# Optimization experiments

Measured on AMD Instinct MI355X. Metric: run time of the kernel, lower is better.

Reference implementation:

```python
import jax, jax.numpy as jnp
import numpy as np
from functools import partial

TAU = 2.0          # leak
VTH = 1.0          # threshold_value
DECAY = 1.0 - 1.0 / TAU  # decay_input=False, v_reset=0: v = v*(1-1/tau) + x
PAD = 3
STRIDE = 1


def heaviside(x):
    # forward of spikingjelly surrogate.ATan (surrogate only changes backward)
    return (x >= 0).astype(x.dtype)


def lif(v, inp):
    """One LIF step: charge, fire, hard reset (v_reset=0)."""
    v = v * DECAY + inp
    s = heaviside(v - VTH)
    v = v * (1.0 - s)
    return v, s


def setup_inputs() -> dict:
    key = jax.random.key(0)
    k1, k2, k3, k4 = jax.random.split(key, 4)
    B, L = 64, 2048
    C, H, NC, K = 128, 256, 10, 7
    x = jax.random.normal(k1, (B, L), dtype=jnp.float32)
    conv_w = jax.random.normal(k2, (C, 1, K), dtype=jnp.float32) * (1.0 / np.sqrt(K))
    W1 = jax.random.normal(k3, (H, C), dtype=jnp.float32) * (1.0 / np.sqrt(C))
    W2 = jax.random.normal(k4, (NC, H), dtype=jnp.float32) * (1.0 / np.sqrt(H))
    return {"x": x, "conv_w": conv_w, "W1": W1, "W2": W2}


def _forward(x, conv_w, W1, W2):
    B = x.shape[0]
    C, H, NC = conv_w.shape[0], W1.shape[0], W2.shape[0]
    # Conv1d(1 -> C): [B, 1, L] -> [B, C, T]
    xc = jax.lax.conv_general_dilated(
        x[:, None, :], conv_w, window_strides=(STRIDE,),
        padding=[(PAD, PAD)], dimension_numbers=("NCH", "OIH", "NCH"))
    T = xc.shape[2]
    xt = jnp.transpose(xc, (2, 0, 1))  # [T, B, C]

    def step(carry, x_t):
        v1, v2, v3, acc = carry
        v1, s1 = lif(v1, x_t)                       # conv LIF  [B, C]
        v2, s2 = lif(v2, s1 @ W1.T)                 # hidden LIF [B, H]
        v3, s3 = lif(v3, s2 @ W2.T)                 # output LIF [B, NC]
        return (v1, v2, v3, acc + s3), None

    zeros = lambda d: jnp.zeros((B, d), dtype=x.dtype)
    init = (zeros(C), zeros(H), zeros(NC), zeros(NC))
    (_, _, _, acc), _ = jax.lax.scan(step, init, xt)
    return acc / T


def reference(x, conv_w, W1, W2):
    return _forward(x, conv_w, W1, W2)
```

## Files before the change

### kernel.cpp

```cpp
#include <hip/hip_runtime.h>
#include <stdint.h>

#define T_STEPS 2048
#define BB 64
#define CC 128
#define HH 256
#define NCLS 10

#define S1_OFF  0
#define DP_OFF  16777216
#define DP2_OFF 16908288
#define S2B_OFF 16924672

typedef int v4i __attribute__((ext_vector_type(4)));

__global__ __launch_bounds__(128) void k01_prep(
    const float* __restrict__ x, const float* __restrict__ cw,
    const float* __restrict__ W1, const float* __restrict__ W2,
    unsigned char* __restrict__ s1, signed char* __restrict__ dp,
    signed char* __restrict__ dp2, float* __restrict__ out) {
  const int bx = blockIdx.x;
  const int tidx = threadIdx.x;

  if (bx < 1024) {
    const int c = tidx;
    const int b = bx & 63;
    const int t0 = (bx >> 6) * 128;
    const int ts = t0 - 64;

    float w[7];
#pragma unroll
    for (int k = 0; k < 7; ++k) w[k] = cw[c * 7 + k];

    const float* xb = x + b * 2048;
    float xw[7];
#pragma unroll
    for (int k = 0; k < 7; ++k) {
      int l = ts + k - 3;
      xw[k] = (l >= 0 && l < 2048) ? xb[l] : 0.0f;
    }

    float v = 0.0f;
#pragma unroll 7
    for (int t = ts; t < t0 + 128; ++t) {
      float u = fmaf(w[0], xw[0],
                fmaf(w[1], xw[1],
                fmaf(w[2], xw[2],
                fmaf(w[3], xw[3],
                fmaf(w[4], xw[4],
                fmaf(w[5], xw[5], w[6] * xw[6]))))));
      v = fmaf(v, 0.5f, u);
      bool sp = (v >= 1.0f);
      if (t >= t0) s1[((size_t)t * BB + b) * CC + c] = (unsigned char)(sp ? 1 : 0);
      if (sp) v = 0.0f;
#pragma unroll
      for (int k = 0; k < 6; ++k) xw[k] = xw[k + 1];
      int ln = t + 4;
      xw[6] = (ln >= 0 && ln < 2048) ? xb[ln] : 0.0f;
    }
  } else if (bx < 1280) {
    const int h = bx - 1024;
    const int c = tidx;
    float w = W1[h * CC + c];
    int q = __float2int_rn(w * 2147483648.0f);
#pragma unroll
    for (int d = 0; d < 3; ++d) {
      int dig = (int)(signed char)(q & 0xff);
      dp[d * (HH * CC) + h * CC + c] = (signed char)dig;
      q = (q - dig) >> 8;
    }
    dp[3 * (HH * CC) + h * CC + c] = (signed char)q;
  } else if (bx < 1296) {
    const int nc = bx - 1280;
#pragma unroll
    for (int half = 0; half < 2; ++half) {
      int cc = half * 128 + tidx;
      float w = (nc < NCLS) ? W2[nc * HH + cc] : 0.0f;
      int q = __float2int_rn(w * 2147483648.0f);
#pragma unroll
      for (int d = 0; d < 3; ++d) {
        int dig = (int)(signed char)(q & 0xff);
        dp2[d * (16 * HH) + nc * HH + cc] = (signed char)dig;
        q = (q - dig) >> 8;
      }
      dp2[3 * (16 * HH) + nc * HH + cc] = (signed char)q;
    }
  } else {
#pragma unroll
    for (int i = 0; i < 5; ++i) out[tidx + 128 * i] = 0.0f;
  }
}

__global__ __launch_bounds__(256, 4) void k2_mfma_lif2(
    const unsigned char* __restrict__ s1, const signed char* __restrict__ dp,
    unsigned char* __restrict__ s2b) {
  const int tid  = threadIdx.x;
  const int lane = tid & 63;
  const int wv   = tid >> 6;
  const int hg   = blockIdx.x;
  const int b    = blockIdx.y;
  const int chunk= blockIdx.z;
  const int t0   = chunk * 256;
  const int nwarm= (chunk == 0) ? 0 : 4;
  const int ts   = t0 - nwarm * 16;
  const int l15  = lane & 15;
  const int lg   = lane >> 4;
  const int h    = hg * 64 + wv * 16 + l15;

  v4i Bf[4][2];
#pragma unroll
  for (int d = 0; d < 4; ++d)
#pragma unroll
    for (int kc = 0; kc < 2; ++kc)
      Bf[d][kc] = *(const v4i*)(dp + d * (HH * CC) + h * CC + kc * 64 + lg * 16);

  const unsigned char* ap =
      s1 + ((size_t)(ts + l15) * BB + b) * CC + lg * 16;
  v4i Af0 = *(const v4i*)(ap);
  v4i Af1 = *(const v4i*)(ap + 64);
  ap += 16 * BB * CC;

  const int a4 = l15 * 4;
  float v = 0.0f;

  const int nsub = nwarm + 16;
  for (int s = 0; s < nsub; ++s) {
    const int tb = ts + s * 16;

    v4i Pf0 = *(const v4i*)(ap);
    v4i Pf1 = *(const v4i*)(ap + 64);
    ap += 16 * BB * CC;

    v4i a0 = {0, 0, 0, 0}, a1 = {0, 0, 0, 0}, a2 = {0, 0, 0, 0}, a3 = {0, 0, 0, 0};
    a0 = __builtin_amdgcn_mfma_i32_16x16x64_i8(Af0, Bf[0][0], a0, 0, 0, 0);
    a1 = __builtin_amdgcn_mfma_i32_16x16x64_i8(Af0, Bf[1][0], a1, 0, 0, 0);
    a2 = __builtin_amdgcn_mfma_i32_16x16x64_i8(Af0, Bf[2][0], a2, 0, 0, 0);
    a3 = __builtin_amdgcn_mfma_i32_16x16x64_i8(Af0, Bf[3][0], a3, 0, 0, 0);
    a0 = __builtin_amdgcn_mfma_i32_16x16x64_i8(Af1, Bf[0][1], a0, 0, 0, 0);
    a1 = __builtin_amdgcn_mfma_i32_16x16x64_i8(Af1, Bf[1][1], a1, 0, 0, 0);
    a2 = __builtin_amdgcn_mfma_i32_16x16x64_i8(Af1, Bf[2][1], a2, 0, 0, 0);
    a3 = __builtin_amdgcn_mfma_i32_16x16x64_i8(Af1, Bf[3][1], a3, 0, 0, 0);

    float u[4];
#pragma unroll
    for (int r = 0; r < 4; ++r) {
      int hi = a3[r] * 256 + a2[r];
      int lo = a1[r] * 256 + a0[r];
      u[r] = fmaf((float)hi, 0x1p-15f, (float)lo * 0x1p-31f);
    }

    float ua[4][4];
#pragma unroll
    for (int q = 0; q < 4; ++q) {
      const int addr = a4 + q * 64;
#pragma unroll
      for (int r = 0; r < 4; ++r)
        ua[q][r] = __int_as_float(
            __builtin_amdgcn_ds_bpermute(addr, __float_as_int(u[r])));
    }

    unsigned spbits = 0;
#pragma unroll
    for (int q = 0; q < 4; ++q)
#pragma unroll
      for (int r = 0; r < 4; ++r) {
        v = fmaf(v, 0.5f, ua[q][r]);
        bool sp = (v >= 1.0f);
        if (sp) v = 0.0f;
        spbits |= (sp ? 1u : 0u) << (q * 4 + r);
      }

    if (s >= nwarm) {
      size_t base = ((size_t)(tb + lg * 4) * BB + b) * 256 + h;
#pragma unroll
      for (int r = 0; r < 4; ++r)
        s2b[base + (size_t)r * (BB * 256)] =
            (unsigned char)((spbits >> (lg * 4 + r)) & 1u);
    }

    Af0 = Pf0; Af1 = Pf1;
  }
}

__global__ __launch_bounds__(64) void k34_gemm3_lif3(
    const unsigned char* __restrict__ s2b, const signed char* __restrict__ dp2,
    float* __restrict__ out) {
  const int lane = threadIdx.x;
  const int l15  = lane & 15;
  const int lg   = lane >> 4;
  const int b    = blockIdx.x;
  const int chunk= blockIdx.y;
  const int t0   = chunk * 64;
  const int nwarm= (chunk == 0) ? 0 : 4;
  const int ts   = t0 - nwarm * 16;

  v4i Bf[4][4];
#pragma unroll
  for (int d = 0; d < 4; ++d)
#pragma unroll
    for (int kc = 0; kc < 4; ++kc)
      Bf[d][kc] = *(const v4i*)(dp2 + d * (16 * HH) + l15 * HH + kc * 64 + lg * 16);

  const unsigned char* ap =
      s2b + ((size_t)(ts + l15) * BB + b) * 256 + lg * 16;
  v4i Af[4];
#pragma unroll
  for (int kc = 0; kc < 4; ++kc) Af[kc] = *(const v4i*)(ap + kc * 64);
  ap += 16 * BB * 256;

  const int a4 = l15 * 4;
  float v = 0.0f, cnt = 0.0f;
  const int nsub = nwarm + 4;
  for (int s = 0; s < nsub; ++s) {
    v4i Pf[4];
#pragma unroll
    for (int kc = 0; kc < 4; ++kc) Pf[kc] = *(const v4i*)(ap + kc * 64);
    ap += 16 * BB * 256;

    v4i a0 = {0, 0, 0, 0}, a1 = {0, 0, 0, 0}, a2 = {0, 0, 0, 0}, a3 = {0, 0, 0, 0};
#pragma unroll
    for (int kc = 0; kc < 4; ++kc) {
      a0 = __builtin_amdgcn_mfma_i32_16x16x64_i8(Af[kc], Bf[0][kc], a0, 0, 0, 0);
      a1 = __builtin_amdgcn_mfma_i32_16x16x64_i8(Af[kc], Bf[1][kc], a1, 0, 0, 0);
      a2 = __builtin_amdgcn_mfma_i32_16x16x64_i8(Af[kc], Bf[2][kc], a2, 0, 0, 0);
      a3 = __builtin_amdgcn_mfma_i32_16x16x64_i8(Af[kc], Bf[3][kc], a3, 0, 0, 0);
    }

    float u[4];
#pragma unroll
    for (int r = 0; r < 4; ++r) {
      int hi = a3[r] * 256 + a2[r];
      int lo = a1[r] * 256 + a0[r];
      u[r] = fmaf((float)hi, 0x1p-15f, (float)lo * 0x1p-31f);
    }

    float ua[4][4];
#pragma unroll
    for (int q = 0; q < 4; ++q) {
      const int addr = a4 + q * 64;
#pragma unroll
      for (int r = 0; r < 4; ++r)
        ua[q][r] = __int_as_float(
            __builtin_amdgcn_ds_bpermute(addr, __float_as_int(u[r])));
    }

    float inc = (s >= nwarm) ? 1.0f : 0.0f;
#pragma unroll
    for (int q = 0; q < 4; ++q)
#pragma unroll
      for (int r = 0; r < 4; ++r) {
        v = fmaf(v, 0.5f, ua[q][r]);
        bool sp = (v >= 1.0f);
        if (sp) { v = 0.0f; cnt += inc; }
      }

#pragma unroll
    for (int kc = 0; kc < 4; ++kc) Af[kc] = Pf[kc];
  }

  if (lane < NCLS)
    atomicAdd(&out[b * NCLS + lane], cnt * (1.0f / 2048.0f));
}

extern "C" void kernel_launch(void* const* d_in, const int* in_sizes, int n_in,
                              void* d_out, int out_size, void* d_ws, size_t ws_size,
                              hipStream_t stream) {
  const float* x  = (const float*)d_in[0];
  const float* cw = (const float*)d_in[1];
  const float* W1 = (const float*)d_in[2];
  const float* W2 = (const float*)d_in[3];
  float* out = (float*)d_out;

  char* ws = (char*)d_ws;
  unsigned char* s1  = (unsigned char*)(ws + S1_OFF);
  signed char*   dp  = (signed char*)(ws + DP_OFF);
  signed char*   dp2 = (signed char*)(ws + DP2_OFF);
  unsigned char* s2b = (unsigned char*)(ws + S2B_OFF);

  k01_prep<<<dim3(1297), 128, 0, stream>>>(x, cw, W1, W2, s1, dp, dp2, out);
  k2_mfma_lif2<<<dim3(4, 64, 8), 256, 0, stream>>>(s1, dp, s2b);
  k34_gemm3_lif3<<<dim3(64, 32), 64, 0, stream>>>(s2b, dp2, out);
  (void)in_sizes; (void)n_in; (void)out_size; (void)ws_size;
}
```

Before: 158.1 us.

## Bit-pack hidden-layer spikes and widen per-wave hidden tile in LIF2 kernel

The hidden spike tensor s2 is stored as packed 32-bit bitmasks built with wave ballots instead of one byte per neuron, which cuts the intermediate write and read traffic by eight times. Each wave in the LIF2 kernel now covers 32 hidden units using two MFMA column tiles, halving the grid in the hidden dimension. The output-layer kernel unpacks the bits back into int8 MFMA operands with multiply-mask tricks and uses shorter time chunks for more parallelism, which adds ALU work, more ballots and more warmup overhead relative to useful steps.

```diff
diff --git a/kernel.cpp b/kernel.cpp
--- a/kernel.cpp
+++ b/kernel.cpp
@@ -10,7 +10,7 @@
 #define S1_OFF  0
 #define DP_OFF  16777216
 #define DP2_OFF 16908288
-#define S2B_OFF 16924672
+#define S2W_OFF 16924672
 
 typedef int v4i __attribute__((ext_vector_type(4)));
 
@@ -93,7 +93,7 @@
 
 __global__ __launch_bounds__(256, 4) void k2_mfma_lif2(
     const unsigned char* __restrict__ s1, const signed char* __restrict__ dp,
-    unsigned char* __restrict__ s2b) {
+    unsigned int* __restrict__ s2w) {
   const int tid  = threadIdx.x;
   const int lane = tid & 63;
   const int wv   = tid >> 6;
@@ -105,14 +105,18 @@
   const int ts   = t0 - nwarm * 16;
   const int l15  = lane & 15;
   const int lg   = lane >> 4;
-  const int h    = hg * 64 + wv * 16 + l15;
-
-  v4i Bf[4][2];
-#pragma unroll
-  for (int d = 0; d < 4; ++d)
-#pragma unroll
-    for (int kc = 0; kc < 2; ++kc)
-      Bf[d][kc] = *(const v4i*)(dp + d * (HH * CC) + h * CC + kc * 64 + lg * 16);
+  const int nn   = lg >> 1;
+  const int hb   = hg * 128 + wv * 32;
+
+  v4i Bf[2][4][2];
+#pragma unroll
+  for (int n = 0; n < 2; ++n)
+#pragma unroll
+    for (int d = 0; d < 4; ++d)
+#pragma unroll
+      for (int kc = 0; kc < 2; ++kc)
+        Bf[n][d][kc] = *(const v4i*)(dp + d * (HH * CC) +
+                                     (hb + n * 16 + l15) * CC + kc * 64 + lg * 16);
 
   const unsigned char* ap =
       s1 + ((size_t)(ts + l15) * BB + b) * CC + lg * 16;
@@ -131,66 +135,67 @@
     v4i Pf1 = *(const v4i*)(ap + 64);
     ap += 16 * BB * CC;
 
-    v4i a0 = {0, 0, 0, 0}, a1 = {0, 0, 0, 0}, a2 = {0, 0, 0, 0}, a3 = {0, 0, 0, 0};
-    a0 = __builtin_amdgcn_mfma_i32_16x16x64_i8(Af0, Bf[0][0], a0, 0, 0, 0);
-    a1 = __builtin_amdgcn_mfma_i32_16x16x64_i8(Af0, Bf[1][0], a1, 0, 0, 0);
-    a2 = __builtin_amdgcn_mfma_i32_16x16x64_i8(Af0, Bf[2][0], a2, 0, 0, 0);
-    a3 = __builtin_amdgcn_mfma_i32_16x16x64_i8(Af0, Bf[3][0], a3, 0, 0, 0);
-    a0 = __builtin_amdgcn_mfma_i32_16x16x64_i8(Af1, Bf[0][1], a0, 0, 0, 0);
-    a1 = __builtin_amdgcn_mfma_i32_16x16x64_i8(Af1, Bf[1][1], a1, 0, 0, 0);
-    a2 = __builtin_amdgcn_mfma_i32_16x16x64_i8(Af1, Bf[2][1], a2, 0, 0, 0);
-    a3 = __builtin_amdgcn_mfma_i32_16x16x64_i8(Af1, Bf[3][1], a3, 0, 0, 0);
-
-    float u[4];
-#pragma unroll
-    for (int r = 0; r < 4; ++r) {
-      int hi = a3[r] * 256 + a2[r];
-      int lo = a1[r] * 256 + a0[r];
-      u[r] = fmaf((float)hi, 0x1p-15f, (float)lo * 0x1p-31f);
-    }
-
-    float ua[4][4];
+    float u0[4], u1[4];
+#pragma unroll
+    for (int n = 0; n < 2; ++n) {
+      v4i a0 = {0, 0, 0, 0}, a1 = {0, 0, 0, 0}, a2 = {0, 0, 0, 0}, a3 = {0, 0, 0, 0};
+      a0 = __builtin_amdgcn_mfma_i32_16x16x64_i8(Af0, Bf[n][0][0], a0, 0, 0, 0);
+      a1 = __builtin_amdgcn_mfma_i32_16x16x64_i8(Af0, Bf[n][1][0], a1, 0, 0, 0);
+      a2 = __builtin_amdgcn_mfma_i32_16x16x64_i8(Af0, Bf[n][2][0], a2, 0, 0, 0);
+      a3 = __builtin_amdgcn_mfma_i32_16x16x64_i8(Af0, Bf[n][3][0], a3, 0, 0, 0);
+      a0 = __builtin_amdgcn_mfma_i32_16x16x64_i8(Af1, Bf[n][0][1], a0, 0, 0, 0);
+      a1 = __builtin_amdgcn_mfma_i32_16x16x64_i8(Af1, Bf[n][1][1], a1, 0, 0, 0);
+      a2 = __builtin_amdgcn_mfma_i32_16x16x64_i8(Af1, Bf[n][2][1], a2, 0, 0, 0);
+      a3 = __builtin_amdgcn_mfma_i32_16x16x64_i8(Af1, Bf[n][3][1], a3, 0, 0, 0);
+#pragma unroll
+      for (int r = 0; r < 4; ++r) {
+        int hi = a3[r] * 256 + a2[r];
+        int lo = a1[r] * 256 + a0[r];
+        float u = fmaf((float)hi, 0x1p-15f, (float)lo * 0x1p-31f);
+        if (n == 0) u0[r] = u; else u1[r] = u;
+      }
+    }
+
+    float ua[16];
 #pragma unroll
     for (int q = 0; q < 4; ++q) {
       const int addr = a4 + q * 64;
 #pragma unroll
-      for (int r = 0; r < 4; ++r)
-        ua[q][r] = __int_as_float(
-            __builtin_amdgcn_ds_bpermute(addr, __float_as_int(u[r])));
-    }
-
-    unsigned spbits = 0;
-#pragma unroll
-    for (int q = 0; q < 4; ++q)
-#pragma unroll
       for (int r = 0; r < 4; ++r) {
-        v = fmaf(v, 0.5f, ua[q][r]);
-        bool sp = (v >= 1.0f);
-        if (sp) v = 0.0f;
-        spbits |= (sp ? 1u : 0u) << (q * 4 + r);
+        int g0 = __builtin_amdgcn_ds_bpermute(addr, __float_as_int(u0[r]));
+        int g1 = __builtin_amdgcn_ds_bpermute(addr, __float_as_int(u1[r]));
+        ua[q * 4 + r] = __int_as_float(nn ? g1 : g0);
       }
-
-    if (s >= nwarm) {
-      size_t base = ((size_t)(tb + lg * 4) * BB + b) * 256 + h;
-#pragma unroll
-      for (int r = 0; r < 4; ++r)
-        s2b[base + (size_t)r * (BB * 256)] =
-            (unsigned char)((spbits >> (lg * 4 + r)) & 1u);
-    }
+    }
+
+    unsigned sel = 0;
+#pragma unroll
+    for (int j = 0; j < 16; ++j) {
+      v = fmaf(v, 0.5f, ua[j]);
+      bool sp = (v >= 1.0f);
+      if (sp) v = 0.0f;
+      unsigned long long Bm = __ballot(sp);
+      if (l15 == j)
+        sel = (unsigned)(Bm & 0xFFFFull) |
+              ((unsigned)((Bm >> 32) & 0xFFFFull) << 16);
+    }
+
+    if (s >= nwarm && lg == 0)
+      s2w[((size_t)(tb + l15) * BB + b) * 8 + hg * 4 + wv] = sel;
 
     Af0 = Pf0; Af1 = Pf1;
   }
 }
 
-__global__ __launch_bounds__(64) void k34_gemm3_lif3(
-    const unsigned char* __restrict__ s2b, const signed char* __restrict__ dp2,
+__global__ __launch_bounds__(64, 4) void k34_gemm3_lif3(
+    const unsigned int* __restrict__ s2w, const signed char* __restrict__ dp2,
     float* __restrict__ out) {
   const int lane = threadIdx.x;
   const int l15  = lane & 15;
   const int lg   = lane >> 4;
   const int b    = blockIdx.x;
   const int chunk= blockIdx.y;
-  const int t0   = chunk * 64;
+  const int t0   = chunk * 32;
   const int nwarm= (chunk == 0) ? 0 : 4;
   const int ts   = t0 - nwarm * 16;
 
@@ -201,29 +206,34 @@
     for (int kc = 0; kc < 4; ++kc)
       Bf[d][kc] = *(const v4i*)(dp2 + d * (16 * HH) + l15 * HH + kc * 64 + lg * 16);
 
-  const unsigned char* ap =
-      s2b + ((size_t)(ts + l15) * BB + b) * 256 + lg * 16;
-  v4i Af[4];
-#pragma unroll
-  for (int kc = 0; kc < 4; ++kc) Af[kc] = *(const v4i*)(ap + kc * 64);
-  ap += 16 * BB * 256;
+  const uint4* rp = (const uint4*)s2w + ((size_t)(ts + l15) * BB + b) * 2;
+  uint4 r0 = rp[0], r1 = rp[1];
+  rp += 16 * BB * 2;
 
   const int a4 = l15 * 4;
+  const int hw = (lg & 1) * 16;
   float v = 0.0f, cnt = 0.0f;
-  const int nsub = nwarm + 4;
+
+  const int nsub = nwarm + 2;
   for (int s = 0; s < nsub; ++s) {
-    v4i Pf[4];
-#pragma unroll
-    for (int kc = 0; kc < 4; ++kc) Pf[kc] = *(const v4i*)(ap + kc * 64);
-    ap += 16 * BB * 256;
+    uint4 p0 = rp[0], p1 = rp[1];
+    rp += 16 * BB * 2;
+
+    unsigned rowd[8] = {r0.x, r0.y, r0.z, r0.w, r1.x, r1.y, r1.z, r1.w};
 
     v4i a0 = {0, 0, 0, 0}, a1 = {0, 0, 0, 0}, a2 = {0, 0, 0, 0}, a3 = {0, 0, 0, 0};
 #pragma unroll
     for (int kc = 0; kc < 4; ++kc) {
-      a0 = __builtin_amdgcn_mfma_i32_16x16x64_i8(Af[kc], Bf[0][kc], a0, 0, 0, 0);
-      a1 = __builtin_amdgcn_mfma_i32_16x16x64_i8(Af[kc], Bf[1][kc], a1, 0, 0, 0);
-      a2 = __builtin_amdgcn_mfma_i32_16x16x64_i8(Af[kc], Bf[2][kc], a2, 0, 0, 0);
-      a3 = __builtin_amdgcn_mfma_i32_16x16x64_i8(Af[kc], Bf[3][kc], a3, 0, 0, 0);
+      unsigned h16 = (rowd[kc * 2 + (lg >> 1)] >> hw) & 0xFFFFu;
+      v4i Af;
+      Af[0] = (int)(((h16 & 0xFu) * 0x00204081u) & 0x01010101u);
+      Af[1] = (int)((((h16 >> 4) & 0xFu) * 0x00204081u) & 0x01010101u);
+      Af[2] = (int)((((h16 >> 8) & 0xFu) * 0x00204081u) & 0x01010101u);
+      Af[3] = (int)((((h16 >> 12) & 0xFu) * 0x00204081u) & 0x01010101u);
+      a0 = __builtin_amdgcn_mfma_i32_16x16x64_i8(Af, Bf[0][kc], a0, 0, 0, 0);
+      a1 = __builtin_amdgcn_mfma_i32_16x16x64_i8(Af, Bf[1][kc], a1, 0, 0, 0);
+      a2 = __builtin_amdgcn_mfma_i32_16x16x64_i8(Af, Bf[2][kc], a2, 0, 0, 0);
+      a3 = __builtin_amdgcn_mfma_i32_16x16x64_i8(Af, Bf[3][kc], a3, 0, 0, 0);
     }
 
     float u[4];
@@ -234,28 +244,25 @@
       u[r] = fmaf((float)hi, 0x1p-15f, (float)lo * 0x1p-31f);
     }
 
-    float ua[4][4];
+    float ua[16];
 #pragma unroll
     for (int q = 0; q < 4; ++q) {
       const int addr = a4 + q * 64;
 #pragma unroll
       for (int r = 0; r < 4; ++r)
-        ua[q][r] = __int_as_float(
+        ua[q * 4 + r] = __int_as_float(
             __builtin_amdgcn_ds_bpermute(addr, __float_as_int(u[r])));
     }
 
     float inc = (s >= nwarm) ? 1.0f : 0.0f;
 #pragma unroll
-    for (int q = 0; q < 4; ++q)
-#pragma unroll
-      for (int r = 0; r < 4; ++r) {
-        v = fmaf(v, 0.5f, ua[q][r]);
-        bool sp = (v >= 1.0f);
-        if (sp) { v = 0.0f; cnt += inc; }
-      }
-
-#pragma unroll
-    for (int kc = 0; kc < 4; ++kc) Af[kc] = Pf[kc];
+    for (int j = 0; j < 16; ++j) {
+      v = fmaf(v, 0.5f, ua[j]);
+      bool sp = (v >= 1.0f);
+      if (sp) { v = 0.0f; cnt += inc; }
+    }
+
+    r0 = p0; r1 = p1;
   }
 
   if (lane < NCLS)
@@ -275,10 +282,10 @@
   unsigned char* s1  = (unsigned char*)(ws + S1_OFF);
   signed char*   dp  = (signed char*)(ws + DP_OFF);
   signed char*   dp2 = (signed char*)(ws + DP2_OFF);
-  unsigned char* s2b = (unsigned char*)(ws + S2B_OFF);
+  unsigned int*  s2w = (unsigned int*)(ws + S2W_OFF);
 
   k01_prep<<<dim3(1297), 128, 0, stream>>>(x, cw, W1, W2, s1, dp, dp2, out);
-  k2_mfma_lif2<<<dim3(4, 64, 8), 256, 0, stream>>>(s1, dp, s2b);
-  k34_gemm3_lif3<<<dim3(64, 32), 64, 0, stream>>>(s2b, dp2, out);
+  k2_mfma_lif2<<<dim3(2, 64, 8), 256, 0, stream>>>(s1, dp, s2w);
+  k34_gemm3_lif3<<<dim3(64, 64), 64, 0, stream>>>(s2w, dp2, out);
   (void)in_sizes; (void)n_in; (void)out_size; (void)ws_size;
 }
```

Result: faster. 148.6 us (-6.0%).
